# Performance work log

Hardware: AMD Instinct MI355X
Metric: run time of the kernel (lower is better)

The kernel has to match this reference:

```python
import jax, jax.numpy as jnp
import numpy as np

LN_EPS = 1e-3  # keras LayerNormalization default epsilon
LEAKY_SLOPE = 0.2  # tf 'leaky_relu' default alpha


def layer_norm(x, gamma, beta):
    mu = jnp.mean(x, axis=-1, keepdims=True)
    var = jnp.mean(jnp.square(x - mu), axis=-1, keepdims=True)
    return (x - mu) * jax.lax.rsqrt(var + LN_EPS) * gamma + beta


def attention_head(q_in, kv_in, Wk, Wv, Wq, causal):
    # q_in: [b, sq, d], kv_in: [b, sk, d]
    K = jnp.einsum('bsd,de->bse', kv_in, Wk)
    V = jnp.einsum('bsd,de->bse', kv_in, Wv)
    Q = jnp.einsum('bsd,de->bse', q_in, Wq)
    sk = K.shape[1]
    # NOTE: original scales by sqrt(window_size_keys), i.e. key seq length
    scores = jnp.einsum('bqe,bke->bqk', Q, K) / jnp.sqrt(jnp.float32(sk))
    if causal:
        sq = Q.shape[1]
        mask = jnp.triu(jnp.full((sq, sk), -jnp.inf, dtype=scores.dtype), k=1)
        scores = scores + mask
    probs = jax.nn.softmax(scores, axis=-1)
    return jnp.einsum('bqk,bke->bqe', probs, V)


def setup_inputs() -> dict:
    key = jax.random.key(0)
    ks = jax.random.split(key, 12)
    B, S, D, H = 4, 4096, 256, 400
    p = lambda k, shp: jax.random.normal(k, shp, dtype=jnp.float32) * 0.1
    return {
        'inputs': jax.random.normal(ks[0], (B, S, D), dtype=jnp.float32),
        'context_sequence': jax.random.normal(ks[1], (B, S, D), dtype=jnp.float32),
        'sa_Wk': p(ks[2], (D, D)),
        'sa_Wv': p(ks[3], (D, D)),
        'sa_Wq': p(ks[4], (D, D)),
        'ca_Wk': p(ks[5], (D, D)),
        'ca_Wv': p(ks[6], (D, D)),
        'ca_Wq': p(ks[7], (D, D)),
        'W1': p(ks[8], (D, H)),
        'b1': jnp.zeros((H,), dtype=jnp.float32),
        'W2': p(ks[9], (H, D)),
        'b2': jnp.zeros((D,), dtype=jnp.float32),
        'gamma': jnp.ones((D,), dtype=jnp.float32),
        'beta': jnp.zeros((D,), dtype=jnp.float32),
    }


def reference(inputs, context_sequence, sa_Wk, sa_Wv, sa_Wq, ca_Wk, ca_Wv, ca_Wq,
              W1, b1, W2, b2, gamma, beta):
    # 1) masked self-attention + residual + LN (shared LN params)
    in_attn = attention_head(inputs, inputs, sa_Wk, sa_Wv, sa_Wq, causal=True)
    x = layer_norm(in_attn + inputs, gamma, beta)
    # 2) unmasked cross-attention (queries = x, keys/values = context) + residual + LN
    ctx_attn = attention_head(x, context_sequence, ca_Wk, ca_Wv, ca_Wq, causal=False)
    y = layer_norm(ctx_attn + x, gamma, beta)
    # 3) FFN (Dense 400 leaky_relu -> Dense emb) + residual + LN
    h = jax.nn.leaky_relu(jnp.einsum('bsd,dh->bsh', y, W1) + b1, negative_slope=LEAKY_SLOPE)
    ff = jnp.einsum('bsh,hd->bsd', h, W2) + b2
    return layer_norm(ff + y, gamma, beta)
```

## Files before the change

kernel.cpp:

```cpp
#include <hip/hip_runtime.h>

typedef __bf16  bf16x4 __attribute__((ext_vector_type(4)));
typedef __bf16  bf16x8 __attribute__((ext_vector_type(8)));
typedef float   f32x4  __attribute__((ext_vector_type(4)));
typedef unsigned int u32;

constexpr int BM = 128, BN = 128, BK = 32;

__device__ __forceinline__ void async_cp16(const __bf16* g, __bf16* lds) {
    __builtin_amdgcn_global_load_lds(
        (const __attribute__((address_space(1))) u32*)g,
        (__attribute__((address_space(3))) u32*)lds, 16, 0, 0);
}

__device__ __forceinline__ int swz(int row, int q) {
    return row * BK + (((q + (row >> 1)) & 3) << 3);
}

template<int EPI>
__launch_bounds__(256)
__global__ void gemm_nt(const __bf16* __restrict__ Aall, const __bf16* __restrict__ Ball,
                        const float* __restrict__ bias,
                        void* __restrict__ C0, void* __restrict__ C1, void* __restrict__ C2,
                        int N, int K, long ldb, long sA, long sB, long sC,
                        int nTx, int klen, long pstrideB)
{
    const int bx = blockIdx.x;
    const int chunk = bx / nTx;
    const int n0 = (bx - chunk * nTx) * BN;
    const int m0 = blockIdx.y * BM;
    const int bz = blockIdx.z;
    const int kbase = chunk * klen;

    const __bf16* A  = Aall + (long)bz * sA;
    const __bf16* Bt = Ball + (long)bz * sB;

    __shared__ alignas(16) __bf16 As[2][BM * BK];
    __shared__ alignas(16) __bf16 Bs[2][BN * BK];

    const int tid = threadIdx.x;
    const int wave = tid >> 6, lane = tid & 63;
    const int wm = (wave >> 1) * 64, wn = (wave & 1) * 64;
    const int quad = lane >> 4, l16 = lane & 15;

    const int row0 = tid >> 2, sl0 = tid & 3;
    const int ks0 = (sl0 - (row0 >> 1)) & 3;
    const int row1 = row0 + 64;
    const int ks1 = (sl0 - (row1 >> 1)) & 3;
    const __bf16* gA0 = A  + (long)(m0 + row0) * K + kbase + ks0 * 8;
    const __bf16* gA1 = A  + (long)(m0 + row1) * K + kbase + ks1 * 8;
    const __bf16* gB0 = Bt + (long)(n0 + row0) * ldb + kbase + ks0 * 8;
    const __bf16* gB1 = Bt + (long)(n0 + row1) * ldb + kbase + ks1 * 8;

    f32x4 acc[4][4];
    #pragma unroll
    for (int i = 0; i < 4; i++)
        #pragma unroll
        for (int j = 0; j < 4; j++) { f32x4 z = {0.f, 0.f, 0.f, 0.f}; acc[i][j] = z; }

    auto stageg = [&](int buf) {
        async_cp16(gA0, As[buf] + wave * 512);
        async_cp16(gA1, As[buf] + 2048 + wave * 512);
        async_cp16(gB0, Bs[buf] + wave * 512);
        async_cp16(gB1, Bs[buf] + 2048 + wave * 512);
        gA0 += BK; gA1 += BK; gB0 += BK; gB1 += BK;
    };

    stageg(0);
    int cur = 0;
    for (int kk = 0; kk < klen; kk += BK) {
        __syncthreads();
        if (kk + BK < klen) stageg(cur ^ 1);

        bf16x8 af[4], bg[4];
        #pragma unroll
        for (int i = 0; i < 4; i++) {
            af[i] = *(const bf16x8*)(As[cur] + swz(wm + i * 16 + l16, quad));
            bg[i] = *(const bf16x8*)(Bs[cur] + swz(wn + i * 16 + l16, quad));
        }
        #pragma unroll
        for (int i = 0; i < 4; i++)
            #pragma unroll
            for (int j = 0; j < 4; j++)
                acc[i][j] = __builtin_amdgcn_mfma_f32_16x16x32_bf16(af[i], bg[j], acc[i][j], 0, 0, 0);
        cur ^= 1;
    }

    char* cb = (char*)C0 + (EPI == 3 ? (long)chunk * pstrideB : 0);
    #pragma unroll
    for (int j = 0; j < 4; j++) {
        const int col = n0 + wn + j * 16 + l16;
        const float bv = (EPI == 2) ? bias[col] : 0.f;
        #pragma unroll
        for (int i = 0; i < 4; i++) {
            #pragma unroll
            for (int r = 0; r < 4; r++) {
                const int row = m0 + wm + i * 16 + quad * 4 + r;
                float c = acc[i][j][r];
                if (EPI == 2) { c += bv; c = c > 0.f ? c : 0.2f * c; }
                if (EPI == 1 || EPI == 3)
                    ((__bf16*)cb)[(long)bz * sC + (long)row * N + col] = (__bf16)c;
                else if (EPI == 2)
                    ((__bf16*)cb)[(long)row * N + col] = (__bf16)c;
                else {
                    const int seg = col >> 8;
                    __bf16* dst = seg == 0 ? (__bf16*)C0 : (seg == 1 ? (__bf16*)C1 : (__bf16*)C2);
                    dst[(long)row * 256 + (col & 255)] = (__bf16)c;
                }
            }
        }
    }
}

template<int CAUSAL>
__launch_bounds__(512, 4)
__global__ void fattn(const __bf16* __restrict__ Qall, const __bf16* __restrict__ Kall,
                      const __bf16* __restrict__ Vt,
                      __bf16* __restrict__ pbuf, float* __restrict__ side,
                      int NS, long pstrideE, float scale)
{
    constexpr int S = 4096, D = 256, R = 16384;
    const int mt = CAUSAL ? (int)(gridDim.x - 1 - blockIdx.x) : (int)blockIdx.x;
    const int chunk = blockIdx.y;
    const int bz = blockIdx.z;
    const int m0 = mt * 64;

    const int T = CAUSAL ? ((m0 + 64) >> 5) : (S >> 5);
    const int t0 = chunk * T / NS;
    const int t1 = (chunk + 1) * T / NS;
    const int kbase = t0 << 5;
    const int ntile = t1 - t0;

    const __bf16* Q  = Qall + ((long)bz * S + m0) * D;
    const __bf16* Kp = Kall + (long)bz * S * D;
    const long vcol0 = (long)bz * S;

    __shared__ alignas(16) __bf16 Ks[2][8192];
    __shared__ alignas(16) __bf16 Vs[2][8192];
    __shared__ alignas(16) __bf16 Ps[64 * 32];
    __shared__ float sred[8][16];

    const int tid = threadIdx.x;
    const int wave = tid >> 6, lane = tid & 63;
    const int quad = lane >> 4, l16 = lane & 15;
    const int wq16 = (wave >> 1) * 16;
    const int wk16 = (wave & 1) * 16;
    const int qh = wave >> 2;
    const int eq = wave & 3;

    bf16x8 qf[8];
    #pragma unroll
    for (int kd = 0; kd < 8; kd++)
        qf[kd] = *(const bf16x8*)(Q + (long)(wq16 + l16) * D + kd * 32 + quad * 8);

    const int srowK = (tid >> 2) & 31;
    const int srowV = tid >> 2;
    const int ks8 = (((tid & 3) - (tid >> 3)) & 3) << 3;
    const int wbase = (tid & ~63) * 8;

    f32x4 acc[2][4];
    #pragma unroll
    for (int i = 0; i < 2; i++)
        #pragma unroll
        for (int j = 0; j < 4; j++) { f32x4 z = {0.f, 0.f, 0.f, 0.f}; acc[i][j] = z; }
    float se[4] = {0.f, 0.f, 0.f, 0.f};

    auto stage = [&](int buf, int kb) {
        const __bf16* gK = Kp + (long)(kb + srowK) * D + ks8 + ((tid >> 7) << 5);
        async_cp16(gK,       Ks[buf] + wbase);
        async_cp16(gK + 128, Ks[buf] + 4096 + wbase);
        const __bf16* gV = Vt + vcol0 + kb + ks8 + (long)srowV * R;
        async_cp16(gV,                 Vs[buf] + wbase);
        async_cp16(gV + (long)128 * R, Vs[buf] + 4096 + wbase);
    };

    if (ntile > 0) stage(0, kbase);

    for (int t = 0; t < ntile; ++t) {
        const int cur = t & 1;
        const int kb = kbase + (t << 5);
        __syncthreads();
        if (t + 1 < ntile) stage(cur ^ 1, kb + 32);

        const __bf16* Kb_ = Ks[cur];
        const __bf16* Vb_ = Vs[cur];

        f32x4 sa = {0.f, 0.f, 0.f, 0.f}, sb = {0.f, 0.f, 0.f, 0.f};
        #pragma unroll
        for (int kd = 0; kd < 4; kd++) {
            bf16x8 b0 = *(const bf16x8*)(Kb_ + kd * 1024 + swz(wk16 + l16, quad));
            bf16x8 b1 = *(const bf16x8*)(Kb_ + (kd + 4) * 1024 + swz(wk16 + l16, quad));
            sa = __builtin_amdgcn_mfma_f32_16x16x32_bf16(qf[kd], b0, sa, 0, 0, 0);
            sb = __builtin_amdgcn_mfma_f32_16x16x32_bf16(qf[kd + 4], b1, sb, 0, 0, 0);
        }

        const bool diag = CAUSAL && (kb >= m0);
        const int kloc = wk16 + l16;
        #pragma unroll
        for (int r = 0; r < 4; r++) {
            const int qloc = wq16 + quad * 4 + r;
            float e = __expf((sa[r] + sb[r]) * scale);
            if (diag && kb + kloc > m0 + qloc) e = 0.f;
            se[r] += e;
            Ps[qloc * 32 + (((kloc >> 3) ^ ((qloc >> 1) & 3)) << 3) + (kloc & 7)] = (__bf16)e;
        }
        __syncthreads();

        {
            const int q0 = qh * 32 + l16;
            const int q1 = q0 + 16;
            const int sx = ((quad ^ ((q0 >> 1) & 3)) << 3);
            bf16x8 pa0 = *(const bf16x8*)(Ps + q0 * 32 + sx);
            bf16x8 pa1 = *(const bf16x8*)(Ps + q1 * 32 + sx);
            #pragma unroll
            for (int j = 0; j < 4; j++) {
                bf16x8 vb = *(const bf16x8*)(Vb_ + swz(eq * 64 + j * 16 + l16, quad));
                acc[0][j] = __builtin_amdgcn_mfma_f32_16x16x32_bf16(pa0, vb, acc[0][j], 0, 0, 0);
                acc[1][j] = __builtin_amdgcn_mfma_f32_16x16x32_bf16(pa1, vb, acc[1][j], 0, 0, 0);
            }
        }
    }

    #pragma unroll
    for (int st = 1; st < 16; st <<= 1)
        #pragma unroll
        for (int r = 0; r < 4; r++) se[r] += __shfl_xor(se[r], st);
    if (l16 == 0)
        #pragma unroll
        for (int r = 0; r < 4; r++)
            sred[wave][quad * 4 + r] = se[r];
    __syncthreads();
    if ((wave & 1) == 0 && l16 == 0) {
        float* sd = side + ((long)bz * 64 + chunk) * 4096 + m0 + wq16;
        #pragma unroll
        for (int r = 0; r < 4; r++) {
            const int idx = quad * 4 + r;
            sd[idx] = sred[wave][idx] + sred[wave + 1][idx];
        }
    }

    __bf16* cb = pbuf + (long)chunk * pstrideE + ((long)bz * S + m0) * D;
    #pragma unroll
    for (int j = 0; j < 4; j++) {
        const int col = eq * 64 + j * 16 + l16;
        #pragma unroll
        for (int i = 0; i < 2; i++)
            #pragma unroll
            for (int r = 0; r < 4; r++)
                cb[(long)(qh * 32 + i * 16 + quad * 4 + r) * D + col] = (__bf16)acc[i][j][r];
    }
}

template<int NP>
__launch_bounds__(256)
__global__ void ln_res(const __bf16* __restrict__ p, long pstr,
                       const float* __restrict__ resid,
                       const float* __restrict__ side, int lim,
                       const float* __restrict__ bias,
                       const float* __restrict__ gamma, const float* __restrict__ beta,
                       float* __restrict__ outf, __bf16* __restrict__ outb)
{
    const int row  = blockIdx.x * 4 + (threadIdx.x >> 6);
    const int lane = threadIdx.x & 63;
    const long vi = (long)row * 64 + lane;
    float p0 = 0.f, p1 = 0.f, p2 = 0.f, p3 = 0.f;
    #pragma unroll
    for (int i = 0; i < NP; i++) {
        bf16x4 vp = ((const bf16x4*)(p + (long)i * pstr))[vi];
        p0 += (float)vp[0]; p1 += (float)vp[1]; p2 += (float)vp[2]; p3 += (float)vp[3];
    }
    if (side) {
        const float* sp = side + (long)(row >> 12) * 64 * 4096 + (row & 4095);
        float sv = 0.f;
        for (int t = 0; t < lim; t++) sv += sp[(long)t * 4096];
        const float iv = 1.f / sv;
        p0 *= iv; p1 *= iv; p2 *= iv; p3 *= iv;
    }
    float4 vr = ((const float4*)resid)[vi];
    float x0 = vr.x + p0, x1 = vr.y + p1, x2 = vr.z + p2, x3 = vr.w + p3;
    if (bias) {
        float4 vb = ((const float4*)bias)[lane];
        x0 += vb.x; x1 += vb.y; x2 += vb.z; x3 += vb.w;
    }
    float s = x0 + x1 + x2 + x3;
    #pragma unroll
    for (int off = 32; off; off >>= 1) s += __shfl_xor(s, off);
    const float mu = s * (1.f / 256.f);
    float d0 = x0 - mu, d1 = x1 - mu, d2 = x2 - mu, d3 = x3 - mu;
    float s2 = d0 * d0 + d1 * d1 + d2 * d2 + d3 * d3;
    #pragma unroll
    for (int off = 32; off; off >>= 1) s2 += __shfl_xor(s2, off);
    const float rs = rsqrtf(s2 * (1.f / 256.f) + 1e-3f);
    const float4 g  = ((const float4*)gamma)[lane];
    const float4 be = ((const float4*)beta)[lane];
    float o0 = d0 * rs * g.x + be.x, o1 = d1 * rs * g.y + be.y;
    float o2 = d2 * rs * g.z + be.z, o3 = d3 * rs * g.w + be.w;
    float4 o; o.x = o0; o.y = o1; o.z = o2; o.w = o3;
    ((float4*)outf)[vi] = o;
    if (outb) {
        bf16x4 ob; ob[0] = (__bf16)o0; ob[1] = (__bf16)o1; ob[2] = (__bf16)o2; ob[3] = (__bf16)o3;
        ((bf16x4*)outb)[vi] = ob;
    }
}

__device__ __forceinline__ void tp(const float* __restrict__ src, __bf16* __restrict__ dst,
                                   int rows, int cols, int rowsP, int i)
{
    const int c = i / rowsP, r = i - c * rowsP;
    const float v = (r < rows && c < cols) ? src[r * cols + c] : 0.f;
    dst[i] = (__bf16)v;
}

__global__ void prep_all(const float4* __restrict__ inA, const float4* __restrict__ inC,
                         bf16x4* __restrict__ outA, bf16x4* __restrict__ outC,
                         const float* __restrict__ sWq, const float* __restrict__ sWk,
                         const float* __restrict__ sWv,
                         const float* __restrict__ cWq, const float* __restrict__ cWk,
                         const float* __restrict__ cWv,
                         const float* __restrict__ W1, const float* __restrict__ W2,
                         __bf16* __restrict__ wqk_s, __bf16* __restrict__ wv_s,
                         __bf16* __restrict__ wq_c, __bf16* __restrict__ wk_c,
                         __bf16* __restrict__ wv_c,
                         __bf16* __restrict__ W1t, __bf16* __restrict__ W2t,
                         const float* __restrict__ b1, float* __restrict__ b1p)
{
    const int bx = blockIdx.x, tid = threadIdx.x;
    if (bx < 8192) {
        const bool a = bx < 4096;
        const long j = (long)(a ? bx : bx - 4096) * 256 + tid;
        float4 v = (a ? inA : inC)[j];
        bf16x4 o; o[0] = (__bf16)v.x; o[1] = (__bf16)v.y; o[2] = (__bf16)v.z; o[3] = (__bf16)v.w;
        (a ? outA : outC)[j] = o;
    }
    else if (bx < 8448)  tp(sWq, wqk_s,          256, 256, 256, (bx - 8192)  * 256 + tid);
    else if (bx < 8704)  tp(sWk, wqk_s + 65536,  256, 256, 256, (bx - 8448)  * 256 + tid);
    else if (bx < 8960)  tp(sWv, wv_s,           256, 256, 256, (bx - 8704)  * 256 + tid);
    else if (bx < 9216)  tp(cWq, wq_c,           256, 256, 256, (bx - 8960)  * 256 + tid);
    else if (bx < 9472)  tp(cWk, wk_c,           256, 256, 256, (bx - 9216)  * 256 + tid);
    else if (bx < 9728)  tp(cWv, wv_c,           256, 256, 256, (bx - 9472)  * 256 + tid);
    else if (bx < 10240) tp(W1,  W1t,            256, 400, 256, (bx - 9728)  * 256 + tid);
    else if (bx < 10752) tp(W2,  W2t,            400, 256, 512, (bx - 10240) * 256 + tid);
    else { const int i = (bx - 10752) * 256 + tid; if (i < 512) b1p[i] = (i < 400) ? b1[i] : 0.f; }
}

extern "C" void kernel_launch(void* const* d_in, const int* in_sizes, int n_in,
                              void* d_out, int out_size, void* d_ws, size_t ws_size,
                              hipStream_t stream)
{
    constexpr int B = 4, S = 4096, D = 256, H = 400, Hp = 512;
    constexpr int R = B * S;
    constexpr float SCALE = 1.f / 64.f;
    constexpr int NSc = 4;
    constexpr int NSx = 2;
    constexpr int NSf = 2;

    const float* inputs = (const float*)d_in[0];
    const float* ctx    = (const float*)d_in[1];
    const float* sa_Wk  = (const float*)d_in[2];
    const float* sa_Wv  = (const float*)d_in[3];
    const float* sa_Wq  = (const float*)d_in[4];
    const float* ca_Wk  = (const float*)d_in[5];
    const float* ca_Wv  = (const float*)d_in[6];
    const float* ca_Wq  = (const float*)d_in[7];
    const float* W1     = (const float*)d_in[8];
    const float* b1     = (const float*)d_in[9];
    const float* W2     = (const float*)d_in[10];
    const float* b2     = (const float*)d_in[11];
    const float* gamma  = (const float*)d_in[12];
    const float* beta   = (const float*)d_in[13];
    float* out = (float*)d_out;

    char* ws = (char*)d_ws;
    size_t off = 0;
    auto alloc = [&](size_t bytes) -> char* {
        char* p = ws + off; off += (bytes + 255) & ~size_t(255); return p;
    };
    __bf16* bfA  = (__bf16*)alloc((size_t)R * D * 2);
    __bf16* bfC  = (__bf16*)alloc((size_t)R * D * 2);
    __bf16* Qb   = (__bf16*)alloc((size_t)R * D * 2);
    __bf16* Kb   = (__bf16*)alloc((size_t)R * D * 2);
    __bf16* Vt   = (__bf16*)alloc((size_t)2 * D * R * 2);
    __bf16* h    = (__bf16*)alloc((size_t)R * Hp * 2);
    float*  x    = (float*)alloc((size_t)R * D * 4);
    float*  y    = (float*)alloc((size_t)R * D * 4);
    float*  side = (float*)alloc((size_t)B * 64 * S * 4);
    __bf16* wqk_s = (__bf16*)alloc((size_t)2 * D * D * 2);
    __bf16* wv_s  = (__bf16*)alloc((size_t)D * D * 2);
    __bf16* wv_c  = (__bf16*)alloc((size_t)D * D * 2);
    __bf16* wq_c  = (__bf16*)alloc((size_t)D * D * 2);
    __bf16* wk_c  = (__bf16*)alloc((size_t)D * D * 2);
    __bf16* W1t  = (__bf16*)alloc((size_t)Hp * D * 2);
    __bf16* W2t  = (__bf16*)alloc((size_t)D * Hp * 2);
    float*  b1p  = (float*)alloc((size_t)Hp * 4);

    const size_t PBb = (size_t)R * D * 2;
    __bf16* pbuf = (__bf16*)alloc((size_t)4 * PBb);
    if (off > ws_size) return;
    const long PBe = (long)R * D;

    __bf16* xbf = bfA;
    __bf16* ybf = bfC;

    const dim3 blk(256);
    const dim3 blk512(512);

    auto launch_ln = [&](int np, const float* res, const float* sd, int lim,
                         const float* bias, float* of, __bf16* ob) {
        if (np == 4)      ln_res<4><<<R / 4, blk, 0, stream>>>(pbuf, PBe, res, sd, lim, bias, gamma, beta, of, ob);
        else if (np == 2) ln_res<2><<<R / 4, blk, 0, stream>>>(pbuf, PBe, res, sd, lim, bias, gamma, beta, of, ob);
        else              ln_res<1><<<R / 4, blk, 0, stream>>>(pbuf, PBe, res, sd, lim, bias, gamma, beta, of, ob);
    };

    prep_all<<<10754, blk, 0, stream>>>((const float4*)inputs, (const float4*)ctx,
        (bf16x4*)bfA, (bf16x4*)bfC, sa_Wq, sa_Wk, sa_Wv, ca_Wq, ca_Wk, ca_Wv, W1, W2,
        wqk_s, wv_s, wq_c, wk_c, wv_c, W1t, W2t, b1, b1p);

    gemm_nt<4><<<dim3(4, 128, 1), blk, 0, stream>>>(bfA, wqk_s, nullptr,
        Qb, Kb, nullptr, 2 * D, D, D, 0, 0, 0, 4, D, 0);
    gemm_nt<1><<<dim3(128, 2, 2), blk, 0, stream>>>(wv_s, bfA, nullptr,
        Vt, nullptr, nullptr, R, D, D, (long)D * D, (long)R * D, (long)D * R, 128, D, 0);

    fattn<1><<<dim3(64, NSc, B), blk512, 0, stream>>>(Qb, Kb, Vt, pbuf, side, NSc, PBe, SCALE);
    launch_ln(NSc, inputs, side, NSc, nullptr, x, xbf);

    gemm_nt<1><<<dim3(2, 128, 2), blk, 0, stream>>>(xbf, wq_c, nullptr,
        Qb, nullptr, nullptr, D, D, D, (long)R * D, (long)D * D, (long)R * D, 2, D, 0);

    fattn<0><<<dim3(64, NSx, B), blk512, 0, stream>>>(Qb, Kb, Vt + (size_t)D * R,
        pbuf, side, NSx, PBe, SCALE);
    launch_ln(NSx, x, side, NSx, nullptr, y, ybf);

    gemm_nt<2><<<dim3(4, 128, 1), blk, 0, stream>>>(ybf, W1t, b1p,
        h, nullptr, nullptr, Hp, D, D, 0, 0, 0, 4, D, 0);
    gemm_nt<3><<<dim3(2 * NSf, 128, 1), blk, 0, stream>>>(h, W2t, nullptr,
        pbuf, nullptr, nullptr, D, Hp, Hp, 0, 0, 0, 2, Hp / NSf, (long)PBb);
    launch_ln(NSf, y, nullptr, 0, b2, out, nullptr);
}
```

Baseline: 395.8 us.

## Software-pipeline attention loop: overlap PV of previous tile with QK of current

Restructures the attention inner loop so the P·V MFMAs for tile t-1 run alongside the QK^T MFMAs for tile t. P is double-buffered and the K and V async loads are split into separate stages. The __syncthreads calls become explicit s_waitcnt plus s_barrier, and a drain step after the loop handles the last tile. It also halves the causal split count (NSc 4→2), which gives fewer, longer chunks and less partial-sum overhead but may cut parallelism.

```diff
diff --git a/kernel.cpp b/kernel.cpp
--- a/kernel.cpp
+++ b/kernel.cpp
@@ -16,6 +16,11 @@
 __device__ __forceinline__ int swz(int row, int q) {
     return row * BK + (((q + (row >> 1)) & 3) << 3);
 }
+
+#define ASM_LGKM0 asm volatile("s_waitcnt lgkmcnt(0)" ::: "memory")
+#define ASM_VM2   asm volatile("s_waitcnt vmcnt(2)" ::: "memory")
+#define ASM_VM0   asm volatile("s_waitcnt vmcnt(0)" ::: "memory")
+#define SBAR()    do { __builtin_amdgcn_s_barrier(); asm volatile("" ::: "memory"); } while (0)
 
 template<int EPI>
 __launch_bounds__(256)
@@ -137,7 +142,7 @@
 
     __shared__ alignas(16) __bf16 Ks[2][8192];
     __shared__ alignas(16) __bf16 Vs[2][8192];
-    __shared__ alignas(16) __bf16 Ps[64 * 32];
+    __shared__ alignas(16) __bf16 Ps[2][2048];
     __shared__ float sred[8][16];
 
     const int tid = threadIdx.x;
@@ -165,26 +170,29 @@
         for (int j = 0; j < 4; j++) { f32x4 z = {0.f, 0.f, 0.f, 0.f}; acc[i][j] = z; }
     float se[4] = {0.f, 0.f, 0.f, 0.f};
 
-    auto stage = [&](int buf, int kb) {
+    auto stageK = [&](int buf, int kb) {
         const __bf16* gK = Kp + (long)(kb + srowK) * D + ks8 + ((tid >> 7) << 5);
         async_cp16(gK,       Ks[buf] + wbase);
         async_cp16(gK + 128, Ks[buf] + 4096 + wbase);
+    };
+    auto stageV = [&](int buf, int kb) {
         const __bf16* gV = Vt + vcol0 + kb + ks8 + (long)srowV * R;
         async_cp16(gV,                 Vs[buf] + wbase);
         async_cp16(gV + (long)128 * R, Vs[buf] + 4096 + wbase);
     };
 
-    if (ntile > 0) stage(0, kbase);
+    const int q0 = qh * 32 + l16;
+    const int q1 = q0 + 16;
+    const int sx = ((quad ^ ((q0 >> 1) & 3)) << 3);
+
+    if (ntile > 0) { stageK(0, kbase); stageV(0, kbase); }
 
     for (int t = 0; t < ntile; ++t) {
         const int cur = t & 1;
         const int kb = kbase + (t << 5);
-        __syncthreads();
-        if (t + 1 < ntile) stage(cur ^ 1, kb + 32);
+        ASM_LGKM0; ASM_VM2; SBAR();
 
         const __bf16* Kb_ = Ks[cur];
-        const __bf16* Vb_ = Vs[cur];
-
         f32x4 sa = {0.f, 0.f, 0.f, 0.f}, sb = {0.f, 0.f, 0.f, 0.f};
         #pragma unroll
         for (int kd = 0; kd < 4; kd++) {
@@ -193,31 +201,47 @@
             sa = __builtin_amdgcn_mfma_f32_16x16x32_bf16(qf[kd], b0, sa, 0, 0, 0);
             sb = __builtin_amdgcn_mfma_f32_16x16x32_bf16(qf[kd + 4], b1, sb, 0, 0, 0);
         }
-
-        const bool diag = CAUSAL && (kb >= m0);
-        const int kloc = wk16 + l16;
-        #pragma unroll
-        for (int r = 0; r < 4; r++) {
-            const int qloc = wq16 + quad * 4 + r;
-            float e = __expf((sa[r] + sb[r]) * scale);
-            if (diag && kb + kloc > m0 + qloc) e = 0.f;
-            se[r] += e;
-            Ps[qloc * 32 + (((kloc >> 3) ^ ((qloc >> 1) & 3)) << 3) + (kloc & 7)] = (__bf16)e;
-        }
-        __syncthreads();
-
-        {
-            const int q0 = qh * 32 + l16;
-            const int q1 = q0 + 16;
-            const int sx = ((quad ^ ((q0 >> 1) & 3)) << 3);
-            bf16x8 pa0 = *(const bf16x8*)(Ps + q0 * 32 + sx);
-            bf16x8 pa1 = *(const bf16x8*)(Ps + q1 * 32 + sx);
+        if (t > 0) {
+            const __bf16* Vb_ = Vs[cur ^ 1];
+            const __bf16* Pp = Ps[cur ^ 1];
+            bf16x8 pa0 = *(const bf16x8*)(Pp + q0 * 32 + sx);
+            bf16x8 pa1 = *(const bf16x8*)(Pp + q1 * 32 + sx);
             #pragma unroll
             for (int j = 0; j < 4; j++) {
                 bf16x8 vb = *(const bf16x8*)(Vb_ + swz(eq * 64 + j * 16 + l16, quad));
                 acc[0][j] = __builtin_amdgcn_mfma_f32_16x16x32_bf16(pa0, vb, acc[0][j], 0, 0, 0);
                 acc[1][j] = __builtin_amdgcn_mfma_f32_16x16x32_bf16(pa1, vb, acc[1][j], 0, 0, 0);
             }
+        }
+        if (t + 1 < ntile) stageK(cur ^ 1, kb + 32);
+        ASM_LGKM0; SBAR();
+
+        if (t + 1 < ntile) stageV(cur ^ 1, kb + 32);
+        const bool diag = CAUSAL && (kb >= m0);
+        const int kloc = wk16 + l16;
+        __bf16* Pw = Ps[cur];
+        #pragma unroll
+        for (int r = 0; r < 4; r++) {
+            const int qloc = wq16 + quad * 4 + r;
+            float e = __expf((sa[r] + sb[r]) * scale);
+            if (diag && kb + kloc > m0 + qloc) e = 0.f;
+            se[r] += e;
+            Pw[qloc * 32 + (((kloc >> 3) ^ ((qloc >> 1) & 3)) << 3) + (kloc & 7)] = (__bf16)e;
+        }
+    }
+
+    if (ntile > 0) {
+        ASM_LGKM0; ASM_VM0; SBAR();
+        const int lb = (ntile - 1) & 1;
+        const __bf16* Vb_ = Vs[lb];
+        const __bf16* Pp = Ps[lb];
+        bf16x8 pa0 = *(const bf16x8*)(Pp + q0 * 32 + sx);
+        bf16x8 pa1 = *(const bf16x8*)(Pp + q1 * 32 + sx);
+        #pragma unroll
+        for (int j = 0; j < 4; j++) {
+            bf16x8 vb = *(const bf16x8*)(Vb_ + swz(eq * 64 + j * 16 + l16, quad));
+            acc[0][j] = __builtin_amdgcn_mfma_f32_16x16x32_bf16(pa0, vb, acc[0][j], 0, 0, 0);
+            acc[1][j] = __builtin_amdgcn_mfma_f32_16x16x32_bf16(pa1, vb, acc[1][j], 0, 0, 0);
         }
     }
 
@@ -350,7 +374,7 @@
     constexpr int B = 4, S = 4096, D = 256, H = 400, Hp = 512;
     constexpr int R = B * S;
     constexpr float SCALE = 1.f / 64.f;
-    constexpr int NSc = 4;
+    constexpr int NSc = 2;
     constexpr int NSx = 2;
     constexpr int NSf = 2;
 
```

Result: faster. 384.1 us (-3.0%).
